# Kernel tuning notes

Hardware: AMD Instinct MI355X
Metric: run time of the kernel (lower is better)

Reference implementation:

```python
import jax, jax.numpy as jnp
import numpy as np

B, N, D, H = 4, 512, 4, 256


def _linear_params(key, fan_in, fan_out):
    # torch.nn.Linear default init: U(-1/sqrt(fan_in), 1/sqrt(fan_in))
    lim = 1.0 / np.sqrt(fan_in)
    kw, kb = jax.random.split(key)
    W = jax.random.uniform(kw, (fan_in, fan_out), minval=-lim, maxval=lim, dtype=jnp.float32)
    b = jax.random.uniform(kb, (fan_out,), minval=-lim, maxval=lim, dtype=jnp.float32)
    return W, b


def setup_inputs() -> dict:
    key = jax.random.key(0)
    ks = jax.random.split(key, 8)
    x = jax.random.normal(ks[0], (B, N, D), dtype=jnp.float32)
    adj = jax.random.uniform(ks[1], (B, N, N), dtype=jnp.float32)  # soft adjacency in [0,1)
    W_e1, b_e1 = _linear_params(ks[2], 2 * D, H)
    W_e2, b_e2 = _linear_params(ks[3], H, H)
    W_n1, b_n1 = _linear_params(ks[4], H, H)
    W_n2, b_n2 = _linear_params(ks[5], H, H)
    W_o1, b_o1 = _linear_params(ks[6], D + H, H)
    W_o, b_o = _linear_params(ks[7], H, D)
    return {
        "x": x, "adj": adj,
        "W_e1": W_e1, "b_e1": b_e1, "W_e2": W_e2, "b_e2": b_e2,
        "W_n1": W_n1, "b_n1": b_n1, "W_n2": W_n2, "b_n2": b_n2,
        "W_o1": W_o1, "b_o1": b_o1, "W_o": W_o, "b_o": b_o,
    }


def reference(x, adj, W_e1, b_e1, W_e2, b_e2, W_n1, b_n1, W_n2, b_n2, W_o1, b_o1, W_o, b_o):
    b_, n_, d_ = x.shape
    # innode[b,i,j,:] = x[b,j]; outnode[b,i,j,:] = x[b,i]
    innode = jnp.broadcast_to(x[:, None, :, :], (b_, n_, n_, d_))
    outnode = jnp.broadcast_to(x[:, :, None, :], (b_, n_, n_, d_))
    edge_in = jnp.concatenate([innode, outnode], axis=-1)          # [B,N,N,2D]
    node2edge = jax.nn.relu(edge_in @ W_e1 + b_e1)                 # [B,N,N,H]
    edge2edge = jax.nn.relu(node2edge @ W_e2 + b_e2)               # [B,N,N,H]
    # adjacency-masked sum over axis 1 (the i axis)
    agg = jnp.einsum('bij,bijh->bjh', adj, edge2edge)              # [B,N,H]
    out1 = jax.nn.relu(agg @ W_n1 + b_n1)
    out2 = jax.nn.relu(out1 @ W_n2 + b_n2)
    out3 = jnp.concatenate([x, out2], axis=-1)                     # [B,N,D+H]
    out4 = out3 @ W_o1 + b_o1
    out5 = out4 @ W_o + b_o                                        # [B,N,D]
    # CONTINUOUS is False for the classifier variant
    return jax.nn.log_softmax(out5, axis=2)
```

## Files before the change

kernel.cpp:

```cpp
#include <hip/hip_runtime.h>
#include <hip/hip_fp16.h>
#include <math.h>

#define Bq 4
#define Nq 512
#define Dq 4
#define Hq 256

typedef _Float16 f16x8 __attribute__((ext_vector_type(8)));
typedef float f32x4 __attribute__((ext_vector_type(4)));

__device__ __forceinline__ f16x8 hadd_relu(f16x8 u, f16x8 v) {
    f16x8 s = u + v;
    const f16x8 z = (f16x8)(_Float16)0.0f;
    return __builtin_elementwise_max(s, z);
}

__device__ __forceinline__ uint4 cvt8h(const float* p) {
    union { __half h[8]; uint4 u; } r;
#pragma unroll
    for (int i = 0; i < 8; ++i) r.h[i] = __float2half(p[i]);
    return r.u;
}

__global__ __launch_bounds__(256) void prep_all(
    const float* __restrict__ x, const float* __restrict__ We1,
    const float* __restrict__ be1, __half* __restrict__ U, __half* __restrict__ V,
    const float* __restrict__ Wn1, const float* __restrict__ Wn2,
    const float* __restrict__ Wo1, __half* __restrict__ Wt16) {
    const int bid = blockIdx.x;
    const int t = threadIdx.x;
    if (bid < 256) {
        const float w0 = We1[0 * 256 + t], w1 = We1[1 * 256 + t];
        const float w2 = We1[2 * 256 + t], w3 = We1[3 * 256 + t];
        const float w4 = We1[4 * 256 + t], w5 = We1[5 * 256 + t];
        const float w6 = We1[6 * 256 + t], w7 = We1[7 * 256 + t];
        const float bv = be1[t];
#pragma unroll
        for (int r = 0; r < 8; ++r) {
            const int row = bid * 8 + r;
            const float* xp = x + row * Dq;
            const float x0 = xp[0], x1 = xp[1], x2 = xp[2], x3 = xp[3];
            float u = bv;
            u = fmaf(x0, w0, u); u = fmaf(x1, w1, u);
            u = fmaf(x2, w2, u); u = fmaf(x3, w3, u);
            float v = x0 * w4;
            v = fmaf(x1, w5, v); v = fmaf(x2, w6, v); v = fmaf(x3, w7, v);
            U[(size_t)row * Hq + t] = __float2half(u);
            V[(size_t)row * Hq + t] = __float2half(v);
        }
    } else {
        __shared__ float ld[64][65];
        const int tid = bid - 256;
        const int mat = tid >> 4;
        const int tile = tid & 15;
        const int k0 = (tile >> 2) * 64;
        const int n0 = (tile & 3) * 64;
        const float* W = (mat == 0) ? Wn1 : (mat == 1) ? Wn2 : (Wo1 + 4 * 256);
        const int rr = t >> 6;
        const int cc = t & 63;
#pragma unroll
        for (int r = 0; r < 16; ++r) {
            const int row = r * 4 + rr;
            ld[row][cc] = W[(size_t)(k0 + row) * 256 + n0 + cc];
        }
        __syncthreads();
#pragma unroll
        for (int r = 0; r < 16; ++r) {
            const int nrow = r * 4 + rr;
            Wt16[((size_t)mat * 256 + n0 + nrow) * 256 + k0 + cc] =
                __float2half(ld[cc][nrow]);
        }
    }
}

__global__ __launch_bounds__(256, 2) void edge_gemm(
    const __half* __restrict__ U, const __half* __restrict__ V,
    const float* __restrict__ We2, const float* __restrict__ be2,
    const float* __restrict__ adj, float* __restrict__ aggws) {
    __shared__ __align__(16) char smem[59392];
    __half* Wt = (__half*)smem;
    __half* Us = (__half*)(smem + 32768);
    __half* Vs = (__half*)(smem + 40960);
    float* adjs = (float*)(smem + 57344);
    float* red = (float*)(smem + 40960);

    const int bid = blockIdx.x;
    const int hq_ = bid & 3;
    const int jt = (bid >> 2) & 31;
    const int b = bid >> 7;
    const int h_base = hq_ * 64;
    const int j_base = jt * 16;
    const int t = threadIdx.x;
    const int lane = t & 63;
    const int w = t >> 6;
    const int q = lane >> 4;
    const int l15 = lane & 15;

    const __half* Vb = V + (size_t)b * Nq * Hq;
    const float* adjb = adj + (size_t)b * Nq * Nq;

    const int srow = t >> 4;
    const int sc0 = (t & 15) * 2;

    {
        const int n = t & 63;
        const int swz = n & 31;
        for (int kk = (t >> 6); kk < 256; kk += 4) {
            float val = We2[kk * 256 + h_base + n];
            Wt[n * 256 + ((((kk >> 3) ^ swz)) << 3) + (kk & 7)] = __float2half(val);
        }
    }
    {
        const uint4* gp = (const uint4*)(U + (size_t)(b * Nq + j_base + srow) * Hq);
        uint4 v0 = gp[sc0];
        uint4 v1 = gp[sc0 + 1];
        *(uint4*)&Us[srow * 256 + ((sc0 ^ srow) << 3)] = v0;
        *(uint4*)&Us[srow * 256 + (((sc0 + 1) ^ srow) << 3)] = v1;
    }

    float bias[4];
#pragma unroll
    for (int nt = 0; nt < 4; ++nt) bias[nt] = be2[h_base + nt * 16 + l15];

    f32x4 agg[4];
#pragma unroll
    for (int nt = 0; nt < 4; ++nt) agg[nt] = (f32x4){0.f, 0.f, 0.f, 0.f};

    uint4 pva, pvb; float pad_;
    {
        const uint4* gp = (const uint4*)(Vb + (size_t)(0 + srow) * Hq);
        pva = gp[sc0]; pvb = gp[sc0 + 1];
        pad_ = adjb[(size_t)(0 + srow) * Nq + j_base + (t & 15)];
        *(uint4*)&Vs[0 * 4096 + srow * 256 + ((sc0 ^ srow) << 3)] = pva;
        *(uint4*)&Vs[0 * 4096 + srow * 256 + (((sc0 + 1) ^ srow) << 3)] = pvb;
        adjs[0 * 256 + t] = pad_;
    }
    {
        const uint4* gp = (const uint4*)(Vb + (size_t)(16 + srow) * Hq);
        pva = gp[sc0]; pvb = gp[sc0 + 1];
        pad_ = adjb[(size_t)(16 + srow) * Nq + j_base + (t & 15)];
    }
    __syncthreads();

    for (int ch = 0; ch < 32; ++ch) {
        const int cur = ch & 1;
        const __half* Vcur = Vs + cur * 4096;
        const float* Acur = adjs + cur * 256;

        f32x4 acc[4][4];
#pragma unroll
        for (int mi = 0; mi < 4; ++mi)
#pragma unroll
            for (int nt = 0; nt < 4; ++nt)
                acc[mi][nt] = (f32x4){bias[nt], bias[nt], bias[nt], bias[nt]};

#pragma unroll
        for (int ks = 0; ks < 8; ++ks) {
            const int c = ks * 4 + q;
            const f16x8 uvec = *(const f16x8*)&Us[l15 * 256 + ((c ^ l15) << 3)];
            f16x8 afrag[4];
#pragma unroll
            for (int mi = 0; mi < 4; ++mi) {
                const int iv = w * 4 + mi;
                const f16x8 vvec = *(const f16x8*)&Vcur[iv * 256 + ((c ^ iv) << 3)];
                afrag[mi] = hadd_relu(uvec, vvec);
            }
            f16x8 bf[4];
#pragma unroll
            for (int nt = 0; nt < 4; ++nt) {
                const int rn = nt * 16 + l15;
                bf[nt] = *(const f16x8*)&Wt[rn * 256 + ((c ^ (rn & 31)) << 3)];
            }
#pragma unroll
            for (int mi = 0; mi < 4; ++mi)
#pragma unroll
                for (int nt = 0; nt < 4; ++nt)
                    acc[mi][nt] = __builtin_amdgcn_mfma_f32_16x16x32_f16(
                        afrag[mi], bf[nt], acc[mi][nt], 0, 0, 0);
        }

#pragma unroll
        for (int mi = 0; mi < 4; ++mi) {
            const int iv = w * 4 + mi;
            const f32x4 av = *(const f32x4*)&Acur[iv * 16 + q * 4];
#pragma unroll
            for (int nt = 0; nt < 4; ++nt) {
                agg[nt][0] = fmaf(av[0], fmaxf(acc[mi][nt][0], 0.f), agg[nt][0]);
                agg[nt][1] = fmaf(av[1], fmaxf(acc[mi][nt][1], 0.f), agg[nt][1]);
                agg[nt][2] = fmaf(av[2], fmaxf(acc[mi][nt][2], 0.f), agg[nt][2]);
                agg[nt][3] = fmaf(av[3], fmaxf(acc[mi][nt][3], 0.f), agg[nt][3]);
            }
        }

        if (ch < 31) {
            const int nxt = cur ^ 1;
            *(uint4*)&Vs[nxt * 4096 + srow * 256 + ((sc0 ^ srow) << 3)] = pva;
            *(uint4*)&Vs[nxt * 4096 + srow * 256 + (((sc0 + 1) ^ srow) << 3)] = pvb;
            adjs[nxt * 256 + t] = pad_;
            if (ch < 30) {
                const int i_base = (ch + 2) * 16;
                const uint4* gp = (const uint4*)(Vb + (size_t)(i_base + srow) * Hq);
                pva = gp[sc0]; pvb = gp[sc0 + 1];
                pad_ = adjb[(size_t)(i_base + srow) * Nq + j_base + (t & 15)];
            }
        }
        __syncthreads();
    }

#pragma unroll
    for (int nt = 0; nt < 4; ++nt)
#pragma unroll
        for (int r = 0; r < 4; ++r)
            red[w * 1024 + (q * 4 + r) * 64 + nt * 16 + l15] = agg[nt][r];
    __syncthreads();
    {
        const int j = t >> 4;
        const int h0 = (t & 15) * 4;
        f32x4 s = *(const f32x4*)&red[0 * 1024 + j * 64 + h0];
        s += *(const f32x4*)&red[1 * 1024 + j * 64 + h0];
        s += *(const f32x4*)&red[2 * 1024 + j * 64 + h0];
        s += *(const f32x4*)&red[3 * 1024 + j * 64 + h0];
        *(f32x4*)&aggws[(size_t)(b * Nq + j_base + j) * Hq + h_base + h0] = s;
    }
}

__global__ __launch_bounds__(256) void tail_kernel(
    const float* __restrict__ aggws, const float* __restrict__ x,
    const __half* __restrict__ Wt16,
    const float* __restrict__ bn1, const float* __restrict__ bn2,
    const float* __restrict__ Wo1, const float* __restrict__ bo1,
    const float* __restrict__ Wo, const float* __restrict__ bo,
    float* __restrict__ out) {
    __shared__ __align__(16) __half actA[16 * 256];
    __shared__ __align__(16) __half actB[16 * 256];
    __shared__ float xs[16][4];
    __shared__ float part[4][16][4];
    __shared__ float s5[16][4];
    const int g0 = blockIdx.x * 16;
    const int t = threadIdx.x;
    const int lane = t & 63;
    const int w = t >> 6;
    const int q = lane >> 4;
    const int l15 = lane & 15;
    const int hb = w * 64;

    {
        const int row = t >> 4;
        const int g = (t & 15) * 2;
        const float* src = aggws + (size_t)(g0 + row) * 256;
        *(uint4*)&actA[row * 256 + ((g ^ row) << 3)] = cvt8h(src + g * 8);
        *(uint4*)&actA[row * 256 + (((g + 1) ^ row) << 3)] = cvt8h(src + g * 8 + 8);
    }
    if (t < 64) xs[t >> 2][t & 3] = x[(size_t)(g0 + (t >> 2)) * 4 + (t & 3)];
    __syncthreads();

    f32x4 acc[4];
#pragma unroll
    for (int nt = 0; nt < 4; ++nt) {
        const float bv = bn1[hb + nt * 16 + l15];
        acc[nt] = (f32x4){bv, bv, bv, bv};
    }
#pragma unroll
    for (int ks = 0; ks < 8; ++ks) {
        const int c = ks * 4 + q;
        const f16x8 af = *(const f16x8*)&actA[l15 * 256 + ((c ^ l15) << 3)];
#pragma unroll
        for (int nt = 0; nt < 4; ++nt) {
            const f16x8 bf = *(const f16x8*)&Wt16[(size_t)(hb + nt * 16 + l15) * 256 + c * 8];
            acc[nt] = __builtin_amdgcn_mfma_f32_16x16x32_f16(af, bf, acc[nt], 0, 0, 0);
        }
    }
#pragma unroll
    for (int nt = 0; nt < 4; ++nt) {
        const int n = hb + nt * 16 + l15;
        const int g = n >> 3;
#pragma unroll
        for (int r = 0; r < 4; ++r) {
            const int row = q * 4 + r;
            actB[row * 256 + ((g ^ row) << 3) + (n & 7)] = __float2half(fmaxf(acc[nt][r], 0.f));
        }
    }
    __syncthreads();

#pragma unroll
    for (int nt = 0; nt < 4; ++nt) {
        const float bv = bn2[hb + nt * 16 + l15];
        acc[nt] = (f32x4){bv, bv, bv, bv};
    }
#pragma unroll
    for (int ks = 0; ks < 8; ++ks) {
        const int c = ks * 4 + q;
        const f16x8 af = *(const f16x8*)&actB[l15 * 256 + ((c ^ l15) << 3)];
#pragma unroll
        for (int nt = 0; nt < 4; ++nt) {
            const f16x8 bf = *(const f16x8*)&Wt16[65536 + (size_t)(hb + nt * 16 + l15) * 256 + c * 8];
            acc[nt] = __builtin_amdgcn_mfma_f32_16x16x32_f16(af, bf, acc[nt], 0, 0, 0);
        }
    }
#pragma unroll
    for (int nt = 0; nt < 4; ++nt) {
        const int n = hb + nt * 16 + l15;
        const int g = n >> 3;
#pragma unroll
        for (int r = 0; r < 4; ++r) {
            const int row = q * 4 + r;
            actA[row * 256 + ((g ^ row) << 3) + (n & 7)] = __float2half(fmaxf(acc[nt][r], 0.f));
        }
    }
    __syncthreads();

#pragma unroll
    for (int nt = 0; nt < 4; ++nt) {
        const int n = hb + nt * 16 + l15;
        const float bv = bo1[n];
        const float w0 = Wo1[0 * 256 + n], w1 = Wo1[1 * 256 + n];
        const float w2 = Wo1[2 * 256 + n], w3 = Wo1[3 * 256 + n];
#pragma unroll
        for (int r = 0; r < 4; ++r) {
            const int row = q * 4 + r;
            float v = bv;
            v = fmaf(xs[row][0], w0, v); v = fmaf(xs[row][1], w1, v);
            v = fmaf(xs[row][2], w2, v); v = fmaf(xs[row][3], w3, v);
            acc[nt][r] = v;
        }
    }
#pragma unroll
    for (int ks = 0; ks < 8; ++ks) {
        const int c = ks * 4 + q;
        const f16x8 af = *(const f16x8*)&actA[l15 * 256 + ((c ^ l15) << 3)];
#pragma unroll
        for (int nt = 0; nt < 4; ++nt) {
            const f16x8 bf = *(const f16x8*)&Wt16[2 * 65536 + (size_t)(hb + nt * 16 + l15) * 256 + c * 8];
            acc[nt] = __builtin_amdgcn_mfma_f32_16x16x32_f16(af, bf, acc[nt], 0, 0, 0);
        }
    }

    float p[4][4];
#pragma unroll
    for (int r = 0; r < 4; ++r)
#pragma unroll
        for (int d = 0; d < 4; ++d) p[r][d] = 0.f;
#pragma unroll
    for (int nt = 0; nt < 4; ++nt) {
        const int n = hb + nt * 16 + l15;
        const float4 wv = *(const float4*)&Wo[n * 4];
#pragma unroll
        for (int r = 0; r < 4; ++r) {
            p[r][0] = fmaf(acc[nt][r], wv.x, p[r][0]);
            p[r][1] = fmaf(acc[nt][r], wv.y, p[r][1]);
            p[r][2] = fmaf(acc[nt][r], wv.z, p[r][2]);
            p[r][3] = fmaf(acc[nt][r], wv.w, p[r][3]);
        }
    }
#pragma unroll
    for (int off = 1; off < 16; off <<= 1)
#pragma unroll
        for (int r = 0; r < 4; ++r)
#pragma unroll
            for (int d = 0; d < 4; ++d)
                p[r][d] += __shfl_xor(p[r][d], off);
    if (l15 == 0) {
#pragma unroll
        for (int r = 0; r < 4; ++r)
#pragma unroll
            for (int d = 0; d < 4; ++d) part[w][q * 4 + r][d] = p[r][d];
    }
    __syncthreads();
    if (t < 64) {
        const int row = t >> 2;
        const int d = t & 3;
        s5[row][d] = part[0][row][d] + part[1][row][d] + part[2][row][d]
                   + part[3][row][d] + bo[d];
    }
    __syncthreads();
    if (t < 16) {
        const float v0 = s5[t][0], v1 = s5[t][1], v2 = s5[t][2], v3 = s5[t][3];
        const float m = fmaxf(fmaxf(v0, v1), fmaxf(v2, v3));
        const float s = expf(v0 - m) + expf(v1 - m) + expf(v2 - m) + expf(v3 - m);
        const float lse = m + logf(s);
        float* op = out + (size_t)(g0 + t) * 4;
        op[0] = v0 - lse; op[1] = v1 - lse; op[2] = v2 - lse; op[3] = v3 - lse;
    }
}

extern "C" void kernel_launch(void* const* d_in, const int* in_sizes, int n_in,
                              void* d_out, int out_size, void* d_ws, size_t ws_size,
                              hipStream_t stream) {
    const float* x   = (const float*)d_in[0];
    const float* adj = (const float*)d_in[1];
    const float* We1 = (const float*)d_in[2];
    const float* be1 = (const float*)d_in[3];
    const float* We2 = (const float*)d_in[4];
    const float* be2 = (const float*)d_in[5];
    const float* Wn1 = (const float*)d_in[6];
    const float* bn1 = (const float*)d_in[7];
    const float* Wn2 = (const float*)d_in[8];
    const float* bn2 = (const float*)d_in[9];
    const float* Wo1 = (const float*)d_in[10];
    const float* bo1 = (const float*)d_in[11];
    const float* Wo  = (const float*)d_in[12];
    const float* bo  = (const float*)d_in[13];
    float* out = (float*)d_out;

    __half* U = (__half*)d_ws;
    __half* V = U + (size_t)Bq * Nq * Hq;
    float* aggws = (float*)((char*)d_ws + (size_t)2 * Bq * Nq * Hq * sizeof(__half));
    __half* Wt16 = (__half*)((char*)d_ws + (size_t)4 * 1024 * 1024);

    prep_all<<<304, 256, 0, stream>>>(x, We1, be1, U, V, Wn1, Wn2, Wo1, Wt16);
    edge_gemm<<<512, 256, 0, stream>>>(U, V, We2, be2, adj, aggws);
    tail_kernel<<<128, 256, 0, stream>>>(aggws, x, Wt16, bn1, bn2, Wo1, bo1, Wo, bo, out);
}
```

Before: 221.9 us.

## Fuse tail MLP into edge_gemm via last-arriving-block atomic tickets

After: 266.8 us. +20.2%, slower.

```diff
diff --git a/kernel.cpp b/kernel.cpp
--- a/kernel.cpp
+++ b/kernel.cpp
@@ -27,7 +27,8 @@
     const float* __restrict__ x, const float* __restrict__ We1,
     const float* __restrict__ be1, __half* __restrict__ U, __half* __restrict__ V,
     const float* __restrict__ Wn1, const float* __restrict__ Wn2,
-    const float* __restrict__ Wo1, __half* __restrict__ Wt16) {
+    const float* __restrict__ Wo1, __half* __restrict__ Wt16,
+    int* __restrict__ counters) {
     const int bid = blockIdx.x;
     const int t = threadIdx.x;
     if (bid < 256) {
@@ -50,6 +51,7 @@
             V[(size_t)row * Hq + t] = __float2half(v);
         }
     } else {
+        if (bid == 256 && t < 128) counters[t] = 0;
         __shared__ float ld[64][65];
         const int tid = bid - 256;
         const int mat = tid >> 4;
@@ -77,8 +79,14 @@
 __global__ __launch_bounds__(256, 2) void edge_gemm(
     const __half* __restrict__ U, const __half* __restrict__ V,
     const float* __restrict__ We2, const float* __restrict__ be2,
-    const float* __restrict__ adj, float* __restrict__ aggws) {
+    const float* __restrict__ adj, float* __restrict__ aggws,
+    const float* __restrict__ x, const __half* __restrict__ Wt16,
+    const float* __restrict__ bn1, const float* __restrict__ bn2,
+    const float* __restrict__ Wo1, const float* __restrict__ bo1,
+    const float* __restrict__ Wo, const float* __restrict__ bo,
+    float* __restrict__ out, int* __restrict__ counters) {
     __shared__ __align__(16) char smem[59392];
+    __shared__ int ticket_s;
     __half* Wt = (__half*)smem;
     __half* Us = (__half*)(smem + 32768);
     __half* Vs = (__half*)(smem + 40960);
@@ -223,164 +231,160 @@
         s += *(const f32x4*)&red[3 * 1024 + j * 64 + h0];
         *(f32x4*)&aggws[(size_t)(b * Nq + j_base + j) * Hq + h_base + h0] = s;
     }
-}
-
-__global__ __launch_bounds__(256) void tail_kernel(
-    const float* __restrict__ aggws, const float* __restrict__ x,
-    const __half* __restrict__ Wt16,
-    const float* __restrict__ bn1, const float* __restrict__ bn2,
-    const float* __restrict__ Wo1, const float* __restrict__ bo1,
-    const float* __restrict__ Wo, const float* __restrict__ bo,
-    float* __restrict__ out) {
-    __shared__ __align__(16) __half actA[16 * 256];
-    __shared__ __align__(16) __half actB[16 * 256];
-    __shared__ float xs[16][4];
-    __shared__ float part[4][16][4];
-    __shared__ float s5[16][4];
-    const int g0 = blockIdx.x * 16;
-    const int t = threadIdx.x;
-    const int lane = t & 63;
-    const int w = t >> 6;
-    const int q = lane >> 4;
-    const int l15 = lane & 15;
-    const int hb = w * 64;
-
-    {
-        const int row = t >> 4;
-        const int g = (t & 15) * 2;
-        const float* src = aggws + (size_t)(g0 + row) * 256;
-        *(uint4*)&actA[row * 256 + ((g ^ row) << 3)] = cvt8h(src + g * 8);
-        *(uint4*)&actA[row * 256 + (((g + 1) ^ row) << 3)] = cvt8h(src + g * 8 + 8);
-    }
-    if (t < 64) xs[t >> 2][t & 3] = x[(size_t)(g0 + (t >> 2)) * 4 + (t & 3)];
+
+    __threadfence();
+    if (t == 0) ticket_s = atomicAdd(&counters[bid >> 2], 1);
     __syncthreads();
-
-    f32x4 acc[4];
-#pragma unroll
-    for (int nt = 0; nt < 4; ++nt) {
-        const float bv = bn1[hb + nt * 16 + l15];
-        acc[nt] = (f32x4){bv, bv, bv, bv};
-    }
-#pragma unroll
-    for (int ks = 0; ks < 8; ++ks) {
-        const int c = ks * 4 + q;
-        const f16x8 af = *(const f16x8*)&actA[l15 * 256 + ((c ^ l15) << 3)];
-#pragma unroll
-        for (int nt = 0; nt < 4; ++nt) {
-            const f16x8 bf = *(const f16x8*)&Wt16[(size_t)(hb + nt * 16 + l15) * 256 + c * 8];
-            acc[nt] = __builtin_amdgcn_mfma_f32_16x16x32_f16(af, bf, acc[nt], 0, 0, 0);
-        }
-    }
-#pragma unroll
-    for (int nt = 0; nt < 4; ++nt) {
-        const int n = hb + nt * 16 + l15;
-        const int g = n >> 3;
-#pragma unroll
-        for (int r = 0; r < 4; ++r) {
-            const int row = q * 4 + r;
-            actB[row * 256 + ((g ^ row) << 3) + (n & 7)] = __float2half(fmaxf(acc[nt][r], 0.f));
-        }
-    }
-    __syncthreads();
-
-#pragma unroll
-    for (int nt = 0; nt < 4; ++nt) {
-        const float bv = bn2[hb + nt * 16 + l15];
-        acc[nt] = (f32x4){bv, bv, bv, bv};
-    }
-#pragma unroll
-    for (int ks = 0; ks < 8; ++ks) {
-        const int c = ks * 4 + q;
-        const f16x8 af = *(const f16x8*)&actB[l15 * 256 + ((c ^ l15) << 3)];
-#pragma unroll
-        for (int nt = 0; nt < 4; ++nt) {
-            const f16x8 bf = *(const f16x8*)&Wt16[65536 + (size_t)(hb + nt * 16 + l15) * 256 + c * 8];
-            acc[nt] = __builtin_amdgcn_mfma_f32_16x16x32_f16(af, bf, acc[nt], 0, 0, 0);
-        }
-    }
-#pragma unroll
-    for (int nt = 0; nt < 4; ++nt) {
-        const int n = hb + nt * 16 + l15;
-        const int g = n >> 3;
-#pragma unroll
-        for (int r = 0; r < 4; ++r) {
-            const int row = q * 4 + r;
-            actA[row * 256 + ((g ^ row) << 3) + (n & 7)] = __float2half(fmaxf(acc[nt][r], 0.f));
-        }
-    }
-    __syncthreads();
-
-#pragma unroll
-    for (int nt = 0; nt < 4; ++nt) {
-        const int n = hb + nt * 16 + l15;
-        const float bv = bo1[n];
-        const float w0 = Wo1[0 * 256 + n], w1 = Wo1[1 * 256 + n];
-        const float w2 = Wo1[2 * 256 + n], w3 = Wo1[3 * 256 + n];
-#pragma unroll
-        for (int r = 0; r < 4; ++r) {
-            const int row = q * 4 + r;
-            float v = bv;
-            v = fmaf(xs[row][0], w0, v); v = fmaf(xs[row][1], w1, v);
-            v = fmaf(xs[row][2], w2, v); v = fmaf(xs[row][3], w3, v);
-            acc[nt][r] = v;
-        }
-    }
-#pragma unroll
-    for (int ks = 0; ks < 8; ++ks) {
-        const int c = ks * 4 + q;
-        const f16x8 af = *(const f16x8*)&actA[l15 * 256 + ((c ^ l15) << 3)];
-#pragma unroll
-        for (int nt = 0; nt < 4; ++nt) {
-            const f16x8 bf = *(const f16x8*)&Wt16[2 * 65536 + (size_t)(hb + nt * 16 + l15) * 256 + c * 8];
-            acc[nt] = __builtin_amdgcn_mfma_f32_16x16x32_f16(af, bf, acc[nt], 0, 0, 0);
-        }
-    }
-
-    float p[4][4];
-#pragma unroll
-    for (int r = 0; r < 4; ++r)
-#pragma unroll
-        for (int d = 0; d < 4; ++d) p[r][d] = 0.f;
-#pragma unroll
-    for (int nt = 0; nt < 4; ++nt) {
-        const int n = hb + nt * 16 + l15;
-        const float4 wv = *(const float4*)&Wo[n * 4];
-#pragma unroll
-        for (int r = 0; r < 4; ++r) {
-            p[r][0] = fmaf(acc[nt][r], wv.x, p[r][0]);
-            p[r][1] = fmaf(acc[nt][r], wv.y, p[r][1]);
-            p[r][2] = fmaf(acc[nt][r], wv.z, p[r][2]);
-            p[r][3] = fmaf(acc[nt][r], wv.w, p[r][3]);
-        }
-    }
-#pragma unroll
-    for (int off = 1; off < 16; off <<= 1)
+    if (ticket_s != 3) return;
+    __threadfence();
+
+    {
+        __half* actA = (__half*)smem;
+        __half* actB = (__half*)(smem + 8192);
+        float* xs = (float*)(smem + 16384);
+        float* part = (float*)(smem + 16640);
+        float* s5 = (float*)(smem + 17664);
+        const int g0 = (bid >> 2) * 16;
+        const int hb = w * 64;
+
+        {
+            const int row = t >> 4;
+            const int g = (t & 15) * 2;
+            const float* src = aggws + (size_t)(g0 + row) * 256;
+            *(uint4*)&actA[row * 256 + ((g ^ row) << 3)] = cvt8h(src + g * 8);
+            *(uint4*)&actA[row * 256 + (((g + 1) ^ row) << 3)] = cvt8h(src + g * 8 + 8);
+        }
+        if (t < 64) xs[(t >> 2) * 4 + (t & 3)] = x[(size_t)(g0 + (t >> 2)) * 4 + (t & 3)];
+        __syncthreads();
+
+        f32x4 acc[4];
+#pragma unroll
+        for (int nt = 0; nt < 4; ++nt) {
+            const float bv = bn1[hb + nt * 16 + l15];
+            acc[nt] = (f32x4){bv, bv, bv, bv};
+        }
+#pragma unroll
+        for (int ks = 0; ks < 8; ++ks) {
+            const int c = ks * 4 + q;
+            const f16x8 af = *(const f16x8*)&actA[l15 * 256 + ((c ^ l15) << 3)];
+#pragma unroll
+            for (int nt = 0; nt < 4; ++nt) {
+                const f16x8 bf = *(const f16x8*)&Wt16[(size_t)(hb + nt * 16 + l15) * 256 + c * 8];
+                acc[nt] = __builtin_amdgcn_mfma_f32_16x16x32_f16(af, bf, acc[nt], 0, 0, 0);
+            }
+        }
+#pragma unroll
+        for (int nt = 0; nt < 4; ++nt) {
+            const int n = hb + nt * 16 + l15;
+            const int g = n >> 3;
+#pragma unroll
+            for (int r = 0; r < 4; ++r) {
+                const int row = q * 4 + r;
+                actB[row * 256 + ((g ^ row) << 3) + (n & 7)] = __float2half(fmaxf(acc[nt][r], 0.f));
+            }
+        }
+        __syncthreads();
+
+#pragma unroll
+        for (int nt = 0; nt < 4; ++nt) {
+            const float bv = bn2[hb + nt * 16 + l15];
+            acc[nt] = (f32x4){bv, bv, bv, bv};
+        }
+#pragma unroll
+        for (int ks = 0; ks < 8; ++ks) {
+            const int c = ks * 4 + q;
+            const f16x8 af = *(const f16x8*)&actB[l15 * 256 + ((c ^ l15) << 3)];
+#pragma unroll
+            for (int nt = 0; nt < 4; ++nt) {
+                const f16x8 bf = *(const f16x8*)&Wt16[65536 + (size_t)(hb + nt * 16 + l15) * 256 + c * 8];
+                acc[nt] = __builtin_amdgcn_mfma_f32_16x16x32_f16(af, bf, acc[nt], 0, 0, 0);
+            }
+        }
+#pragma unroll
+        for (int nt = 0; nt < 4; ++nt) {
+            const int n = hb + nt * 16 + l15;
+            const int g = n >> 3;
+#pragma unroll
+            for (int r = 0; r < 4; ++r) {
+                const int row = q * 4 + r;
+                actA[row * 256 + ((g ^ row) << 3) + (n & 7)] = __float2half(fmaxf(acc[nt][r], 0.f));
+            }
+        }
+        __syncthreads();
+
+#pragma unroll
+        for (int nt = 0; nt < 4; ++nt) {
+            const int n = hb + nt * 16 + l15;
+            const float bv = bo1[n];
+            const float w0 = Wo1[0 * 256 + n], w1 = Wo1[1 * 256 + n];
+            const float w2 = Wo1[2 * 256 + n], w3 = Wo1[3 * 256 + n];
+#pragma unroll
+            for (int r = 0; r < 4; ++r) {
+                const int row = q * 4 + r;
+                float v = bv;
+                v = fmaf(xs[row * 4 + 0], w0, v); v = fmaf(xs[row * 4 + 1], w1, v);
+                v = fmaf(xs[row * 4 + 2], w2, v); v = fmaf(xs[row * 4 + 3], w3, v);
+                acc[nt][r] = v;
+            }
+        }
+#pragma unroll
+        for (int ks = 0; ks < 8; ++ks) {
+            const int c = ks * 4 + q;
+            const f16x8 af = *(const f16x8*)&actA[l15 * 256 + ((c ^ l15) << 3)];
+#pragma unroll
+            for (int nt = 0; nt < 4; ++nt) {
+                const f16x8 bf = *(const f16x8*)&Wt16[2 * 65536 + (size_t)(hb + nt * 16 + l15) * 256 + c * 8];
+                acc[nt] = __builtin_amdgcn_mfma_f32_16x16x32_f16(af, bf, acc[nt], 0, 0, 0);
+            }
+        }
+
+        float p[4][4];
 #pragma unroll
         for (int r = 0; r < 4; ++r)
 #pragma unroll
-            for (int d = 0; d < 4; ++d)
-                p[r][d] += __shfl_xor(p[r][d], off);
-    if (l15 == 0) {
-#pragma unroll
-        for (int r = 0; r < 4; ++r)
-#pragma unroll
-            for (int d = 0; d < 4; ++d) part[w][q * 4 + r][d] = p[r][d];
-    }
-    __syncthreads();
-    if (t < 64) {
-        const int row = t >> 2;
-        const int d = t & 3;
-        s5[row][d] = part[0][row][d] + part[1][row][d] + part[2][row][d]
-                   + part[3][row][d] + bo[d];
-    }
-    __syncthreads();
-    if (t < 16) {
-        const float v0 = s5[t][0], v1 = s5[t][1], v2 = s5[t][2], v3 = s5[t][3];
-        const float m = fmaxf(fmaxf(v0, v1), fmaxf(v2, v3));
-        const float s = expf(v0 - m) + expf(v1 - m) + expf(v2 - m) + expf(v3 - m);
-        const float lse = m + logf(s);
-        float* op = out + (size_t)(g0 + t) * 4;
-        op[0] = v0 - lse; op[1] = v1 - lse; op[2] = v2 - lse; op[3] = v3 - lse;
+            for (int d = 0; d < 4; ++d) p[r][d] = 0.f;
+#pragma unroll
+        for (int nt = 0; nt < 4; ++nt) {
+            const int n = hb + nt * 16 + l15;
+            const float4 wv = *(const float4*)&Wo[n * 4];
+#pragma unroll
+            for (int r = 0; r < 4; ++r) {
+                p[r][0] = fmaf(acc[nt][r], wv.x, p[r][0]);
+                p[r][1] = fmaf(acc[nt][r], wv.y, p[r][1]);
+                p[r][2] = fmaf(acc[nt][r], wv.z, p[r][2]);
+                p[r][3] = fmaf(acc[nt][r], wv.w, p[r][3]);
+            }
+        }
+#pragma unroll
+        for (int off = 1; off < 16; off <<= 1)
+#pragma unroll
+            for (int r = 0; r < 4; ++r)
+#pragma unroll
+                for (int d = 0; d < 4; ++d)
+                    p[r][d] += __shfl_xor(p[r][d], off);
+        if (l15 == 0) {
+#pragma unroll
+            for (int r = 0; r < 4; ++r)
+#pragma unroll
+                for (int d = 0; d < 4; ++d) part[(w * 16 + q * 4 + r) * 4 + d] = p[r][d];
+        }
+        __syncthreads();
+        if (t < 64) {
+            const int row = t >> 2;
+            const int d = t & 3;
+            s5[row * 4 + d] = part[(0 * 16 + row) * 4 + d] + part[(1 * 16 + row) * 4 + d]
+                            + part[(2 * 16 + row) * 4 + d] + part[(3 * 16 + row) * 4 + d] + bo[d];
+        }
+        __syncthreads();
+        if (t < 16) {
+            const float v0 = s5[t * 4 + 0], v1 = s5[t * 4 + 1];
+            const float v2 = s5[t * 4 + 2], v3 = s5[t * 4 + 3];
+            const float m = fmaxf(fmaxf(v0, v1), fmaxf(v2, v3));
+            const float s = expf(v0 - m) + expf(v1 - m) + expf(v2 - m) + expf(v3 - m);
+            const float lse = m + logf(s);
+            float* op = out + (size_t)(g0 + t) * 4;
+            op[0] = v0 - lse; op[1] = v1 - lse; op[2] = v2 - lse; op[3] = v3 - lse;
+        }
     }
 }
 
@@ -407,8 +411,10 @@
     __half* V = U + (size_t)Bq * Nq * Hq;
     float* aggws = (float*)((char*)d_ws + (size_t)2 * Bq * Nq * Hq * sizeof(__half));
     __half* Wt16 = (__half*)((char*)d_ws + (size_t)4 * 1024 * 1024);
-
-    prep_all<<<304, 256, 0, stream>>>(x, We1, be1, U, V, Wn1, Wn2, Wo1, Wt16);
-    edge_gemm<<<512, 256, 0, stream>>>(U, V, We2, be2, adj, aggws);
-    tail_kernel<<<128, 256, 0, stream>>>(aggws, x, Wt16, bn1, bn2, Wo1, bo1, Wo, bo, out);
+    int* counters = (int*)((char*)d_ws + (size_t)4 * 1024 * 1024 + 393216);
+
+    prep_all<<<304, 256, 0, stream>>>(x, We1, be1, U, V, Wn1, Wn2, Wo1, Wt16, counters);
+    edge_gemm<<<512, 256, 0, stream>>>(U, V, We2, be2, adj, aggws,
+                                       x, Wt16, bn1, bn2, Wo1, bo1, Wo, bo,
+                                       out, counters);
 }
```
